# Kernel tuning notes

Measured on AMD Instinct MI355X. Metric: run time of the kernel, lower is better.

The kernel has to match this reference:

```python
import jax, jax.numpy as jnp
import numpy as np
from jax import lax

THR = 0.0
NMS_SIZE = 5
PAD = NMS_SIZE // 2
B, C, H, W = 8, 1, 2048, 2048
# Upper bound on number of surviving peaks: ~1/(2*25) of pixels pass in
# expectation for iid noise; B*H*W//8 is a very safe static cap.
MAX_PEAKS = (B * H * W) // 8


def max_filter(x):
    # torch MaxPool2d(kernel=5, stride=1, padding=2) == max reduce_window
    # with -inf padding, same spatial output shape.
    return lax.reduce_window(
        x, -jnp.inf, lax.max,
        window_dimensions=(1, 1, NMS_SIZE, NMS_SIZE),
        window_strides=(1, 1, 1, 1),
        padding=[(0, 0), (0, 0), (PAD, PAD), (PAD, PAD)],
    )


def setup_inputs() -> dict:
    key = jax.random.key(0)
    scores = jax.random.normal(key, (B, C, H, W), dtype=jnp.float32)
    return {"scores": scores}


def reference(scores):
    # maxima = (scores == maxpool(scores)) & (scores > thr)
    maxima = (scores == max_filter(scores)) & (scores > THR)
    # torch: maxima.nonzero().t()[2:4] -> [2, K] rows = (h, w) coords.
    # jit-safe: fixed-size nonzero, padded with -1 for absent entries.
    idx = jnp.nonzero(maxima, size=MAX_PEAKS, fill_value=-1)
    return jnp.stack([idx[2], idx[3]])  # [2, MAX_PEAKS]
```

## Files before the change

kernel.cpp:

```cpp
#include <hip/hip_runtime.h>
#include <math.h>

#define IMG_W 2048
#define IMG_H 2048
#define BATCH 8
#define MAX_PEAKS ((BATCH * IMG_H * IMG_W) / 8)
#define NWORDS (BATCH * IMG_H * IMG_W / 32)
#define NFILL 2048


#define LOADR(RS, ES)                                                         \
  {                                                                           \
    RS = *(const float4*)p;                                                   \
    const float2 _e = *(const float2*)pe;                                     \
    ES.x = evalid ? _e.x : NEG;                                               \
    ES.y = evalid ? _e.y : NEG;                                               \
    const size_t stepB =                                                      \
        ((unsigned)(xn - 1) < 2047u) ? (size_t)(IMG_W * 4) : (size_t)0;       \
    p = (const float*)((const char*)p + stepB);                               \
    pe = (const float*)((const char*)pe + stepB);                             \
    ++xn;                                                                     \
  }

#define HMR(RS, ES, HS)                                                       \
  {                                                                           \
    float Av = __shfl_up(RS.z, 1);                                            \
    float Bv = __shfl_up(RS.w, 1);                                            \
    float Cv = __shfl_down(RS.x, 1);                                          \
    float Dv = __shfl_down(RS.y, 1);                                          \
    if (isL) { Av = ES.x; Bv = ES.y; }                                        \
    if (isR) { Cv = ES.x; Dv = ES.y; }                                        \
    const float t12 = fmaxf(RS.y, RS.z);                                      \
    const float m02 = fmaxf(RS.x, t12);                                       \
    const float m03 = fmaxf(m02, RS.w);                                       \
    const float m13 = fmaxf(t12, RS.w);                                       \
    HS.x = fmaxf(fmaxf(Av, Bv), m02);                                         \
    HS.y = fmaxf(Bv, m03);                                                    \
    HS.z = fmaxf(m03, Cv);                                                    \
    HS.w = fmaxf(m13, fmaxf(Cv, Dv));                                         \
  }

#define OUTR(MR)                                                              \
  {                                                                           \
    const float mx = fmaxf(fmaxf(fmaxf(H0.x, H1.x), fmaxf(H2.x, H3.x)), H4.x);\
    const float my = fmaxf(fmaxf(fmaxf(H0.y, H1.y), fmaxf(H2.y, H3.y)), H4.y);\
    const float mz = fmaxf(fmaxf(fmaxf(H0.z, H1.z), fmaxf(H2.z, H3.z)), H4.z);\
    const float mw = fmaxf(fmaxf(fmaxf(H0.w, H1.w), fmaxf(H2.w, H3.w)), H4.w);\
    unsigned nib = 0;                                                         \
    nib |= (MR.x > 0.0f && MR.x >= mx) ? 1u : 0u;                             \
    nib |= (MR.y > 0.0f && MR.y >= my) ? 2u : 0u;                             \
    nib |= (MR.z > 0.0f && MR.z >= mz) ? 4u : 0u;                             \
    nib |= (MR.w > 0.0f && MR.w >= mw) ? 8u : 0u;                             \
    unsigned wd = nib << shamt;                                               \
    wd |= __shfl_xor(wd, 1);                                                  \
    wd |= __shfl_xor(wd, 2);                                                  \
    wd |= __shfl_xor(wd, 4);                                                  \
    if ((lane & 7) == 0) {                                                    \
      words[wIdx] = wd;                                                       \
      cnt += __popc(wd);                                                      \
    }                                                                         \
    wIdx += IMG_W / 32;                                                       \
  }

__global__ __launch_bounds__(256, 6) void nms_mask(const float* __restrict__ scores,
                                                   unsigned* __restrict__ words,
                                                   unsigned* __restrict__ bsum2) {
    const int t = threadIdx.x;
    const int lane = t & 63;
    const int wv = t >> 6;
    const int b = blockIdx.x;
    const int L = (b >> 3) + (b & 7) * 256;
    const int img = L >> 8;
    const int rem = L & 255;
    const int strip = rem >> 5;
    const int chunk = rem & 31;
    const int r0 = chunk * 64 + wv * 16;
    const int c0 = strip * 256;
    const int cl = c0 + lane * 4;
    const size_t imgBase = (size_t)img * ((size_t)IMG_H * IMG_W);
    const float NEG = -INFINITY;

    const bool leftHalf = (lane < 32);
    const bool isL = (lane == 0), isR = (lane == 63);
    const int ecol2 = leftHalf ? (c0 - 2) : (c0 + 256);
    const bool evalid = ((unsigned)ecol2 < (unsigned)IMG_W);
    const int ecol2C = evalid ? ecol2 : c0;

    const int rstart = (r0 - 2) < 0 ? 0 : (r0 - 2);
    const float* p = scores + imgBase + (size_t)rstart * IMG_W + cl;
    const float* pe = scores + imgBase + (size_t)rstart * IMG_W + ecol2C;
    int xn = r0 - 1;

    float4 R0, R1, R2, R3;
    float4 H0, H1, H2, H3, H4;
    float2 E0, E1;

    unsigned cnt = 0;
    const int shamt = (lane & 7) * 4;
    size_t wIdx = (size_t)(img * IMG_H + r0) * (IMG_W / 32) + strip * 8 + (lane >> 3);
    const int cb0 = (img * IMG_H + r0) >> 4;

    LOADR(R0, E0);
    LOADR(R1, E1); HMR(R0, E0, H0);
    LOADR(R2, E0); HMR(R1, E1, H1);
    LOADR(R3, E1); HMR(R2, E0, H2);
    LOADR(R0, E0); HMR(R3, E1, H3);
    LOADR(R1, E1); HMR(R0, E0, H4); OUTR(R2);
    LOADR(R2, E0); HMR(R1, E1, H0); OUTR(R3);
    LOADR(R3, E1); HMR(R2, E0, H1); OUTR(R0);
    LOADR(R0, E0); HMR(R3, E1, H2); OUTR(R1);
    LOADR(R1, E1); HMR(R0, E0, H3); OUTR(R2);
    LOADR(R2, E0); HMR(R1, E1, H4); OUTR(R3);
    LOADR(R3, E1); HMR(R2, E0, H0); OUTR(R0);
    LOADR(R0, E0); HMR(R3, E1, H1); OUTR(R1);
    LOADR(R1, E1); HMR(R0, E0, H2); OUTR(R2);
    LOADR(R2, E0); HMR(R1, E1, H3); OUTR(R3);
    LOADR(R3, E1); HMR(R2, E0, H4); OUTR(R0);
    LOADR(R0, E0); HMR(R3, E1, H0); OUTR(R1);
    LOADR(R1, E1); HMR(R0, E0, H1); OUTR(R2);
    LOADR(R2, E0); HMR(R1, E1, H2); OUTR(R3);
    LOADR(R3, E1); HMR(R2, E0, H3); OUTR(R0);
                   HMR(R3, E1, H4); OUTR(R1);

    unsigned s = cnt;
    s += __shfl_xor(s, 1);
    s += __shfl_xor(s, 2);
    s += __shfl_xor(s, 4);
    s += __shfl_xor(s, 8);
    s += __shfl_xor(s, 16);
    s += __shfl_xor(s, 32);
    if (lane == 0) bsum2[cb0 * 8 + strip] = s;
}

__global__ __launch_bounds__(256) void nms_compact(const unsigned* __restrict__ words,
                                                   const unsigned* __restrict__ bsum2,
                                                   int* __restrict__ out) {
    const int t = threadIdx.x;
    const int b = blockIdx.x;
    const int lane = t & 63, wid = t >> 6;
    __shared__ unsigned sred[4];
    __shared__ unsigned wq[4];

    const int limq = ((b < 1024) ? (b * 8) : 8192) >> 2;
    unsigned acc = 0;
    const uint4* p4 = (const uint4*)bsum2;
    for (int i = t; i < limq; i += 256) {
        uint4 a = p4[i];
        acc += a.x + a.y + a.z + a.w;
    }
    acc += __shfl_xor(acc, 1);
    acc += __shfl_xor(acc, 2);
    acc += __shfl_xor(acc, 4);
    acc += __shfl_xor(acc, 8);
    acc += __shfl_xor(acc, 16);
    acc += __shfl_xor(acc, 32);
    if (lane == 0) sred[wid] = acc;
    __syncthreads();
    const unsigned basev = sred[0] + sred[1] + sred[2] + sred[3];

    if (b < 1024) {
        uint4 q = ((const uint4*)(words + b * 1024))[t];
        unsigned wv[4] = {q.x, q.y, q.z, q.w};
        unsigned tsum = __popc(wv[0]) + __popc(wv[1]) + __popc(wv[2]) + __popc(wv[3]);
        unsigned sc = tsum;
#pragma unroll
        for (int d = 1; d < 64; d <<= 1) {
            unsigned o = __shfl_up(sc, d);
            if (lane >= d) sc += o;
        }
        if (lane == 63) wq[wid] = sc;
        __syncthreads();
        unsigned wpre = 0;
#pragma unroll
        for (int k = 0; k < 4; ++k) wpre += (k < wid) ? wq[k] : 0u;
        unsigned off = basev + wpre + sc - tsum;

        const unsigned gword0 = (unsigned)b * 1024u + (unsigned)t * 4u;
#pragma unroll
        for (int wi = 0; wi < 4; ++wi) {
            unsigned m = wv[wi];
            unsigned pbase = (gword0 + wi) << 5;
            while (m) {
                int bit = __builtin_ctz(m);
                m &= m - 1;
                unsigned ppix = pbase + (unsigned)bit;
                int hh = (int)((ppix >> 11) & 2047u);
                int ww = (int)(ppix & 2047u);
                if (off < (unsigned)MAX_PEAKS) {
                    out[off] = hh;
                    out[MAX_PEAKS + off] = ww;
                }
                ++off;
            }
        }
    } else {
        unsigned total = basev;
        if (total > (unsigned)MAX_PEAKS) total = MAX_PEAKS;
        unsigned tail = (unsigned)MAX_PEAKS - total;
        unsigned fb = (unsigned)(b - 1024);
        unsigned per = (tail + NFILL - 1) / NFILL;
        unsigned s = total + fb * per;
        unsigned e = s + per;
        if (s > (unsigned)MAX_PEAKS) s = MAX_PEAKS;
        if (e > (unsigned)MAX_PEAKS) e = MAX_PEAKS;
        unsigned a = (s + 3u) & ~3u;
        if (a > e) a = e;
        unsigned e4 = e & ~3u;
        if (e4 < a) e4 = a;
        if ((unsigned)t < a - s) {
            out[s + t] = -1;
            out[MAX_PEAKS + s + t] = -1;
        }
        const int4 m4 = make_int4(-1, -1, -1, -1);
        for (unsigned k = a / 4 + t; k < e4 / 4; k += 256) {
            ((int4*)out)[k] = m4;
            ((int4*)(out + MAX_PEAKS))[k] = m4;
        }
        if ((unsigned)t < e - e4) {
            out[e4 + t] = -1;
            out[MAX_PEAKS + e4 + t] = -1;
        }
    }
}

extern "C" void kernel_launch(void* const* d_in, const int* in_sizes, int n_in,
                              void* d_out, int out_size, void* d_ws, size_t ws_size,
                              hipStream_t stream) {
    const float* scores = (const float*)d_in[0];
    int* out = (int*)d_out;
    unsigned* words = (unsigned*)d_ws;
    unsigned* bsum2 = words + NWORDS;

    nms_mask<<<2048, 256, 0, stream>>>(scores, words, bsum2);
    nms_compact<<<1024 + NFILL, 256, 0, stream>>>(words, bsum2, out);
}
```

Baseline: 216.7 us.

## Load neighbor float4s directly, transpose mask nibbles, add separate prefix-scan kernel

```diff
diff --git a/kernel.cpp b/kernel.cpp
--- a/kernel.cpp
+++ b/kernel.cpp
@@ -9,60 +9,69 @@
 #define NFILL 2048
 
 
-#define LOADR(RS, ES)                                                         \
-  {                                                                           \
-    RS = *(const float4*)p;                                                   \
-    const float2 _e = *(const float2*)pe;                                     \
-    ES.x = evalid ? _e.x : NEG;                                               \
-    ES.y = evalid ? _e.y : NEG;                                               \
+#define LOAD3(i)                                                              \
+  {                                                                           \
+    q##i##L = *(const float4*)pL;                                             \
+    q##i##M = *(const float4*)pM;                                             \
+    q##i##R = *(const float4*)pR;                                             \
     const size_t stepB =                                                      \
         ((unsigned)(xn - 1) < 2047u) ? (size_t)(IMG_W * 4) : (size_t)0;       \
-    p = (const float*)((const char*)p + stepB);                               \
-    pe = (const float*)((const char*)pe + stepB);                             \
+    pL += stepB;                                                              \
+    pM += stepB;                                                              \
+    pR += stepB;                                                              \
     ++xn;                                                                     \
   }
 
-#define HMR(RS, ES, HS)                                                       \
-  {                                                                           \
-    float Av = __shfl_up(RS.z, 1);                                            \
-    float Bv = __shfl_up(RS.w, 1);                                            \
-    float Cv = __shfl_down(RS.x, 1);                                          \
-    float Dv = __shfl_down(RS.y, 1);                                          \
-    if (isL) { Av = ES.x; Bv = ES.y; }                                        \
-    if (isR) { Cv = ES.x; Dv = ES.y; }                                        \
-    const float t12 = fmaxf(RS.y, RS.z);                                      \
-    const float m02 = fmaxf(RS.x, t12);                                       \
-    const float m03 = fmaxf(m02, RS.w);                                       \
-    const float m13 = fmaxf(t12, RS.w);                                       \
-    HS.x = fmaxf(fmaxf(Av, Bv), m02);                                         \
-    HS.y = fmaxf(Bv, m03);                                                    \
-    HS.z = fmaxf(m03, Cv);                                                    \
-    HS.w = fmaxf(m13, fmaxf(Cv, Dv));                                         \
-  }
-
-#define OUTR(MR)                                                              \
-  {                                                                           \
-    const float mx = fmaxf(fmaxf(fmaxf(H0.x, H1.x), fmaxf(H2.x, H3.x)), H4.x);\
-    const float my = fmaxf(fmaxf(fmaxf(H0.y, H1.y), fmaxf(H2.y, H3.y)), H4.y);\
-    const float mz = fmaxf(fmaxf(fmaxf(H0.z, H1.z), fmaxf(H2.z, H3.z)), H4.z);\
-    const float mw = fmaxf(fmaxf(fmaxf(H0.w, H1.w), fmaxf(H2.w, H3.w)), H4.w);\
+#define COMP(i, HS, MS)                                                       \
+  {                                                                           \
+    const float qlz = fixL ? NEG : q##i##L.z;                                 \
+    const float qlw = fixL ? NEG : q##i##L.w;                                 \
+    const float qrx = fixR ? NEG : q##i##R.x;                                 \
+    const float qry = fixR ? NEG : q##i##R.y;                                 \
+    const float4 qm = q##i##M;                                                \
+    const float ab = fmaxf(qm.x, qm.y);                                       \
+    const float cd = fmaxf(qm.z, qm.w);                                       \
+    const float bc = fmaxf(qm.y, qm.z);                                       \
+    const float abcd = fmaxf(ab, cd);                                         \
+    HS.x = fmaxf(fmaxf(qlz, qlw), fmaxf(ab, qm.z));                           \
+    HS.y = fmaxf(qlw, abcd);                                                  \
+    HS.z = fmaxf(abcd, qrx);                                                  \
+    HS.w = fmaxf(fmaxf(bc, qm.w), fmaxf(qrx, qry));                           \
+    MS = qm;                                                                  \
+  }
+
+#define OUT(MS, pos)                                                          \
+  {                                                                           \
+    const float vx = fmaxf(fmaxf(fmaxf(H0.x, H1.x), fmaxf(H2.x, H3.x)), H4.x);\
+    const float vy = fmaxf(fmaxf(fmaxf(H0.y, H1.y), fmaxf(H2.y, H3.y)), H4.y);\
+    const float vz = fmaxf(fmaxf(fmaxf(H0.z, H1.z), fmaxf(H2.z, H3.z)), H4.z);\
+    const float vw = fmaxf(fmaxf(fmaxf(H0.w, H1.w), fmaxf(H2.w, H3.w)), H4.w);\
     unsigned nib = 0;                                                         \
-    nib |= (MR.x > 0.0f && MR.x >= mx) ? 1u : 0u;                             \
-    nib |= (MR.y > 0.0f && MR.y >= my) ? 2u : 0u;                             \
-    nib |= (MR.z > 0.0f && MR.z >= mz) ? 4u : 0u;                             \
-    nib |= (MR.w > 0.0f && MR.w >= mw) ? 8u : 0u;                             \
-    unsigned wd = nib << shamt;                                               \
-    wd |= __shfl_xor(wd, 1);                                                  \
-    wd |= __shfl_xor(wd, 2);                                                  \
-    wd |= __shfl_xor(wd, 4);                                                  \
-    if ((lane & 7) == 0) {                                                    \
-      words[wIdx] = wd;                                                       \
-      cnt += __popc(wd);                                                      \
-    }                                                                         \
-    wIdx += IMG_W / 32;                                                       \
-  }
-
-__global__ __launch_bounds__(256, 6) void nms_mask(const float* __restrict__ scores,
+    nib |= (MS.x > 0.0f && MS.x >= vx) ? 1u : 0u;                             \
+    nib |= (MS.y > 0.0f && MS.y >= vy) ? 2u : 0u;                             \
+    nib |= (MS.z > 0.0f && MS.z >= vz) ? 4u : 0u;                             \
+    nib |= (MS.w > 0.0f && MS.w >= vw) ? 8u : 0u;                             \
+    bacc |= nib << (4 * (pos));                                               \
+  }
+
+#define MERGE(g)                                                              \
+  {                                                                           \
+    unsigned x = bacc, y;                                                     \
+    y = __shfl_xor(x, 4);                                                     \
+    x = (lane & 4) ? ((y >> 16) | (x & 0xFFFF0000u))                          \
+                   : ((x & 0x0000FFFFu) | (y << 16));                         \
+    y = __shfl_xor(x, 2);                                                     \
+    x = (lane & 2) ? (((y >> 8) & 0x00FF00FFu) | (x & 0xFF00FF00u))           \
+                   : ((x & 0x00FF00FFu) | ((y << 8) & 0xFF00FF00u));          \
+    y = __shfl_xor(x, 1);                                                     \
+    x = (lane & 1) ? (((y >> 4) & 0x0F0F0F0Fu) | (x & 0xF0F0F0F0u))           \
+                   : ((x & 0x0F0F0F0Fu) | ((y << 4) & 0xF0F0F0F0u));          \
+    words[wIdx0 + (g) * 512u] = x;                                            \
+    cnt += __popc(x);                                                         \
+    bacc = 0;                                                                 \
+  }
+
+__global__ __launch_bounds__(256, 4) void nms_mask(const float* __restrict__ scores,
                                                    unsigned* __restrict__ words,
                                                    unsigned* __restrict__ bsum2) {
     const int t = threadIdx.x;
@@ -80,47 +89,46 @@
     const size_t imgBase = (size_t)img * ((size_t)IMG_H * IMG_W);
     const float NEG = -INFINITY;
 
-    const bool leftHalf = (lane < 32);
-    const bool isL = (lane == 0), isR = (lane == 63);
-    const int ecol2 = leftHalf ? (c0 - 2) : (c0 + 256);
-    const bool evalid = ((unsigned)ecol2 < (unsigned)IMG_W);
-    const int ecol2C = evalid ? ecol2 : c0;
+    const bool fixL = (lane == 0) && (strip == 0);
+    const bool fixR = (lane == 63) && (strip == 7);
 
     const int rstart = (r0 - 2) < 0 ? 0 : (r0 - 2);
-    const float* p = scores + imgBase + (size_t)rstart * IMG_W + cl;
-    const float* pe = scores + imgBase + (size_t)rstart * IMG_W + ecol2C;
+    const char* rowp = (const char*)(scores + imgBase + (size_t)rstart * IMG_W);
+    const char* pL = rowp + 4 * (cl - 4) + (fixL ? 16 : 0);
+    const char* pM = rowp + 4 * cl;
+    const char* pR = rowp + 4 * (cl + 4) - (fixR ? 16 : 0);
     int xn = r0 - 1;
 
-    float4 R0, R1, R2, R3;
+    float4 q0L, q0M, q0R, q1L, q1M, q1R, q2L, q2M, q2R, q3L, q3M, q3R;
     float4 H0, H1, H2, H3, H4;
-    float2 E0, E1;
-
-    unsigned cnt = 0;
-    const int shamt = (lane & 7) * 4;
-    size_t wIdx = (size_t)(img * IMG_H + r0) * (IMG_W / 32) + strip * 8 + (lane >> 3);
+    float4 m0, m1, m2;
+
+    unsigned cnt = 0, bacc = 0;
+    const unsigned wIdx0 =
+        (unsigned)(img * IMG_H + r0 + (lane & 7)) * 64u + strip * 8u + (lane >> 3);
     const int cb0 = (img * IMG_H + r0) >> 4;
 
-    LOADR(R0, E0);
-    LOADR(R1, E1); HMR(R0, E0, H0);
-    LOADR(R2, E0); HMR(R1, E1, H1);
-    LOADR(R3, E1); HMR(R2, E0, H2);
-    LOADR(R0, E0); HMR(R3, E1, H3);
-    LOADR(R1, E1); HMR(R0, E0, H4); OUTR(R2);
-    LOADR(R2, E0); HMR(R1, E1, H0); OUTR(R3);
-    LOADR(R3, E1); HMR(R2, E0, H1); OUTR(R0);
-    LOADR(R0, E0); HMR(R3, E1, H2); OUTR(R1);
-    LOADR(R1, E1); HMR(R0, E0, H3); OUTR(R2);
-    LOADR(R2, E0); HMR(R1, E1, H4); OUTR(R3);
-    LOADR(R3, E1); HMR(R2, E0, H0); OUTR(R0);
-    LOADR(R0, E0); HMR(R3, E1, H1); OUTR(R1);
-    LOADR(R1, E1); HMR(R0, E0, H2); OUTR(R2);
-    LOADR(R2, E0); HMR(R1, E1, H3); OUTR(R3);
-    LOADR(R3, E1); HMR(R2, E0, H4); OUTR(R0);
-    LOADR(R0, E0); HMR(R3, E1, H0); OUTR(R1);
-    LOADR(R1, E1); HMR(R0, E0, H1); OUTR(R2);
-    LOADR(R2, E0); HMR(R1, E1, H2); OUTR(R3);
-    LOADR(R3, E1); HMR(R2, E0, H3); OUTR(R0);
-                   HMR(R3, E1, H4); OUTR(R1);
+    LOAD3(0); LOAD3(1); LOAD3(2);
+    LOAD3(3); COMP(0, H0, m0);
+    LOAD3(0); COMP(1, H1, m1);
+    LOAD3(1); COMP(2, H2, m2);
+    LOAD3(2); COMP(3, H3, m0);
+    LOAD3(3); COMP(0, H4, m1); OUT(m2, 0);
+    LOAD3(0); COMP(1, H0, m2); OUT(m0, 1);
+    LOAD3(1); COMP(2, H1, m0); OUT(m1, 2);
+    LOAD3(2); COMP(3, H2, m1); OUT(m2, 3);
+    LOAD3(3); COMP(0, H3, m2); OUT(m0, 4);
+    LOAD3(0); COMP(1, H4, m0); OUT(m1, 5);
+    LOAD3(1); COMP(2, H0, m1); OUT(m2, 6);
+    LOAD3(2); COMP(3, H1, m2); OUT(m0, 7); MERGE(0);
+    LOAD3(3); COMP(0, H2, m0); OUT(m1, 0);
+    LOAD3(0); COMP(1, H3, m1); OUT(m2, 1);
+    LOAD3(1); COMP(2, H4, m2); OUT(m0, 2);
+    LOAD3(2); COMP(3, H0, m0); OUT(m1, 3);
+    LOAD3(3); COMP(0, H1, m1); OUT(m2, 4);
+              COMP(1, H2, m2); OUT(m0, 5);
+              COMP(2, H3, m0); OUT(m1, 6);
+              COMP(3, H4, m1); OUT(m2, 7); MERGE(1);
 
     unsigned s = cnt;
     s += __shfl_xor(s, 1);
@@ -132,33 +140,43 @@
     if (lane == 0) bsum2[cb0 * 8 + strip] = s;
 }
 
+__global__ __launch_bounds__(256) void nms_scan(const unsigned* __restrict__ bsum2,
+                                                unsigned* __restrict__ base) {
+    __shared__ unsigned wtot[4];
+    const int t = threadIdx.x;
+    const int lane = t & 63, wid = t >> 6;
+    const uint4* p = (const uint4*)(bsum2 + t * 32);
+    unsigned c[4];
+#pragma unroll
+    for (int i = 0; i < 4; ++i) {
+        uint4 a = p[2 * i], bq = p[2 * i + 1];
+        c[i] = a.x + a.y + a.z + a.w + bq.x + bq.y + bq.z + bq.w;
+    }
+    unsigned s0 = c[0], s1 = s0 + c[1], s2 = s1 + c[2], ts = s2 + c[3];
+    unsigned sc = ts;
+#pragma unroll
+    for (int d = 1; d < 64; d <<= 1) {
+        unsigned o = __shfl_up(sc, d);
+        if (lane >= d) sc += o;
+    }
+    if (lane == 63) wtot[wid] = sc;
+    __syncthreads();
+    unsigned wpre = 0;
+#pragma unroll
+    for (int k = 0; k < 4; ++k) wpre += (k < wid) ? wtot[k] : 0u;
+    unsigned excl = wpre + sc - ts;
+    ((uint4*)base)[t] = make_uint4(excl, excl + s0, excl + s1, excl + s2);
+    if (t == 255) base[1024] = wpre + sc;
+}
+
 __global__ __launch_bounds__(256) void nms_compact(const unsigned* __restrict__ words,
-                                                   const unsigned* __restrict__ bsum2,
+                                                   const unsigned* __restrict__ base,
                                                    int* __restrict__ out) {
     const int t = threadIdx.x;
     const int b = blockIdx.x;
-    const int lane = t & 63, wid = t >> 6;
-    __shared__ unsigned sred[4];
-    __shared__ unsigned wq[4];
-
-    const int limq = ((b < 1024) ? (b * 8) : 8192) >> 2;
-    unsigned acc = 0;
-    const uint4* p4 = (const uint4*)bsum2;
-    for (int i = t; i < limq; i += 256) {
-        uint4 a = p4[i];
-        acc += a.x + a.y + a.z + a.w;
-    }
-    acc += __shfl_xor(acc, 1);
-    acc += __shfl_xor(acc, 2);
-    acc += __shfl_xor(acc, 4);
-    acc += __shfl_xor(acc, 8);
-    acc += __shfl_xor(acc, 16);
-    acc += __shfl_xor(acc, 32);
-    if (lane == 0) sred[wid] = acc;
-    __syncthreads();
-    const unsigned basev = sred[0] + sred[1] + sred[2] + sred[3];
-
     if (b < 1024) {
+        __shared__ unsigned wq[4];
+        const int lane = t & 63, wid = t >> 6;
         uint4 q = ((const uint4*)(words + b * 1024))[t];
         unsigned wv[4] = {q.x, q.y, q.z, q.w};
         unsigned tsum = __popc(wv[0]) + __popc(wv[1]) + __popc(wv[2]) + __popc(wv[3]);
@@ -173,7 +191,7 @@
         unsigned wpre = 0;
 #pragma unroll
         for (int k = 0; k < 4; ++k) wpre += (k < wid) ? wq[k] : 0u;
-        unsigned off = basev + wpre + sc - tsum;
+        unsigned off = base[b] + wpre + sc - tsum;
 
         const unsigned gword0 = (unsigned)b * 1024u + (unsigned)t * 4u;
 #pragma unroll
@@ -194,7 +212,7 @@
             }
         }
     } else {
-        unsigned total = basev;
+        unsigned total = base[1024];
         if (total > (unsigned)MAX_PEAKS) total = MAX_PEAKS;
         unsigned tail = (unsigned)MAX_PEAKS - total;
         unsigned fb = (unsigned)(b - 1024);
@@ -230,7 +248,9 @@
     int* out = (int*)d_out;
     unsigned* words = (unsigned*)d_ws;
     unsigned* bsum2 = words + NWORDS;
+    unsigned* base = bsum2 + 8192;
 
     nms_mask<<<2048, 256, 0, stream>>>(scores, words, bsum2);
-    nms_compact<<<1024 + NFILL, 256, 0, stream>>>(words, bsum2, out);
-}
+    nms_scan<<<1, 256, 0, stream>>>(bsum2, base);
+    nms_compact<<<1024 + NFILL, 256, 0, stream>>>(words, base, out);
+}
```

New measurement: 216.6 us. No clear change (-0.0%).
